# Kernel tuning notes

Measured on AMD Instinct MI355X. Metric: run time of the kernel, lower is better.

The kernel has to match this reference:

```python
import jax, jax.numpy as jnp
import numpy as np

REL_DIM = 64
HIDDEN = 128
IN_DIM = 7  # dist, dx, dy, color_diff(3), size_diff(1)


def setup_inputs() -> dict:
    key = jax.random.key(0)
    ks = jax.random.split(key, 8)
    B, N = 4, 512
    pos = jax.random.normal(ks[0], (B, N, 2), dtype=jnp.float32)
    color = jax.random.uniform(ks[1], (B, N, 3), dtype=jnp.float32)
    size = jax.random.uniform(ks[2], (B, N, 1), dtype=jnp.float32)
    # MLP params: Linear(7,128) -> GELU -> Linear(128,64), torch default init scale
    W1 = jax.random.normal(ks[3], (IN_DIM, HIDDEN), dtype=jnp.float32) / np.sqrt(IN_DIM)
    b1 = jax.random.normal(ks[4], (HIDDEN,), dtype=jnp.float32) * 0.01
    W2 = jax.random.normal(ks[5], (HIDDEN, REL_DIM), dtype=jnp.float32) / np.sqrt(HIDDEN)
    b2 = jax.random.normal(ks[6], (REL_DIM,), dtype=jnp.float32) * 0.01
    return {"pos": pos, "color": color, "size": size,
            "W1": W1, "b1": b1, "W2": W2, "b2": b2}


def reference(pos, color, size, W1, b1, W2, b2):
    # pos: (B,N,2), color: (B,N,3), size: (B,N,1)
    dx = pos[:, :, None, 0] - pos[:, None, :, 0]          # (B,N,N)
    dy = pos[:, :, None, 1] - pos[:, None, :, 1]          # (B,N,N)
    dist = jnp.sqrt(dx * dx + dy * dy + 1e-6)             # (B,N,N)
    color_diff = color[:, :, None, :] - color[:, None, :, :]  # (B,N,N,3)
    size_diff = size[:, :, None, :] - size[:, None, :, :]     # (B,N,N,1)
    geom = jnp.concatenate(
        [dist[..., None], dx[..., None], dy[..., None], color_diff, size_diff],
        axis=-1)                                          # (B,N,N,7)
    h = jax.nn.gelu(jnp.einsum('bijc,ch->bijh', geom, W1) + b1, approximate=False)
    rel = jnp.einsum('bijh,hr->bijr', h, W2) + b2          # (B,N,N,rel_dim)
    return rel
```

## Files before the change

### kernel.cpp

```cpp
#include <hip/hip_runtime.h>
#include <math.h>

#define NPTS 512
#define HID 128
#define RELD 64

typedef __attribute__((ext_vector_type(8))) short short8;
typedef __attribute__((ext_vector_type(4))) float f32x4;
typedef __attribute__((ext_vector_type(4))) int i32x4;

__global__ __launch_bounds__(256) void prep_tables(
    const float* __restrict__ pos, const float* __restrict__ color,
    const float* __restrict__ size, const float* __restrict__ W1,
    const float* __restrict__ b1, float* __restrict__ ui,
    unsigned short* __restrict__ uj, int npts)
{
  const int g = blockIdx.x * blockDim.x + threadIdx.x;
  const int k = g & (HID - 1), p = g >> 7;
  float v = pos[p * 2 + 0] * W1[1 * HID + k];
  v = fmaf(pos[p * 2 + 1], W1[2 * HID + k], v);
  v = fmaf(color[p * 3 + 0], W1[3 * HID + k], v);
  v = fmaf(color[p * 3 + 1], W1[4 * HID + k], v);
  v = fmaf(color[p * 3 + 2], W1[5 * HID + k], v);
  v = fmaf(size[p], W1[6 * HID + k], v);
  ui[g] = v + b1[k];
  const __bf16 vb = (__bf16)v;
  uj[((size_t)(k >> 3) * npts + p) * 8 + (k & 7)] = __builtin_bit_cast(unsigned short, vb);
}

__global__ __launch_bounds__(256) void relgeom_mfma5(
    const float* __restrict__ pos, const float* __restrict__ W1,
    const float* __restrict__ ui, const unsigned short* __restrict__ uj,
    const float* __restrict__ W2, const float* __restrict__ b2,
    float* __restrict__ out, int npts)
{
  __shared__ __align__(16) char lds[16384 + 4 * 4096];
  const int tid = threadIdx.x;
  const int lane = tid & 63, wid = tid >> 6;
  const int l15 = lane & 15, lq = lane >> 4, l3 = lane & 3;

#pragma unroll
  for (int n = 0; n < 32; ++n) {
    const int m = tid + 256 * n;
    const int k = m >> 6, r = m & 63;
    const __bf16 wb = (__bf16)W2[m];
    *(__bf16*)(lds + r * 256 + (((k >> 3) ^ (r & 7)) << 4) + (k & 7) * 2) = wb;
  }
  __syncthreads();

  const int bx = blockIdx.x;
  const int i  = (bx >> 1) & (NPTS - 1);
  const int b  = bx >> 10;
  const int pi = b * NPTS + i;
  const int j  = ((bx & 1) << 8) + tid;
  const int pj = b * NPTS + j;

  const float dx = pos[pi * 2 + 0] - pos[pj * 2 + 0];
  const float dy = pos[pi * 2 + 1] - pos[pj * 2 + 1];
  const float dist = sqrtf(fmaf(dx, dx, fmaf(dy, dy, 1e-6f)));

  const float* __restrict__ uirow = ui + (size_t)pi * HID;
  const float* __restrict__ w1d = W1;

  f32x4 acc[4][4];
#pragma unroll
  for (int rt = 0; rt < 4; ++rt) {
    const f32x4 bb = *(const f32x4*)(b2 + rt * 16 + lq * 4);
#pragma unroll
    for (int pt = 0; pt < 4; ++pt) acc[rt][pt] = bb;
  }

  char* const hbase = lds + 16384 + wid * 4096;

  for (int ks = 0; ks < 4; ++ks) {
    union { i32x4 v[4]; unsigned u[16]; } U;
#pragma unroll
    for (int d = 0; d < 4; ++d)
      U.v[d] = *(const i32x4*)(uj + ((size_t)(ks * 4 + d) * npts + pj) * 8);

    union { short s[32]; i32x4 v[4]; } hb;
#pragma unroll
    for (int kk = 0; kk < 32; ++kk) {
      const int k = ks * 32 + kk;
      const unsigned w = U.u[kk >> 1];
      const float ujf = __builtin_bit_cast(float, (kk & 1) ? (w & 0xffff0000u) : (w << 16));
      float h = fmaf(dist, w1d[k], uirow[k] - ujf);
      const float h2 = h * h;
      const float wq = fmaf(h2, -0.1029534f, -2.3022077f);
      const float ex = __builtin_amdgcn_exp2f(h * wq);
      const float gel = h * __builtin_amdgcn_rcpf(1.0f + ex);
      const __bf16 hbf = (__bf16)gel;
      hb.s[kk] = __builtin_bit_cast(short, hbf);
    }
#pragma unroll
    for (int d = 0; d < 4; ++d)
      *(i32x4*)(hbase + lane * 64 + ((d ^ l3) << 4)) = hb.v[d];

    short8 afr[4];
#pragma unroll
    for (int rt = 0; rt < 4; ++rt) {
      const int r = rt * 16 + l15;
      afr[rt] = *(const short8*)(lds + r * 256 + (((ks * 4 + lq) ^ (r & 7)) << 4));
    }
#pragma unroll
    for (int pt = 0; pt < 4; ++pt) {
      const int p = pt * 16 + l15;
      const short8 bfr = *(const short8*)(hbase + p * 64 + ((lq ^ (p & 3)) << 4));
#pragma unroll
      for (int rt = 0; rt < 4; ++rt)
        acc[rt][pt] = __builtin_amdgcn_mfma_f32_16x16x32_bf16(afr[rt], bfr, acc[rt][pt], 0, 0, 0);
    }
  }

  const int pbase = bx * 256 + wid * 64;
#pragma unroll
  for (int pt = 0; pt < 4; ++pt) {
#pragma unroll
    for (int rt = 0; rt < 4; ++rt) {
      const int c = (rt * 4 + lq) ^ l15;
      *(f32x4*)(hbase + l15 * 256 + (c & 15) * 16) = acc[rt][pt];
    }
    float* const ob = out + (size_t)(pbase + pt * 16) * RELD;
#pragma unroll
    for (int m = 0; m < 4; ++m) {
      const int g = m * 64 + lane;
      const int pr = g >> 4;
      const int c = (g & 15) ^ pr;
      const f32x4 v = *(const f32x4*)(hbase + pr * 256 + (c & 15) * 16);
      *(f32x4*)(ob + (size_t)g * 4) = v;
    }
  }
}

__global__ __launch_bounds__(256) void relgeom_mfma_fb(
    const float* __restrict__ pos, const float* __restrict__ color,
    const float* __restrict__ size, const float* __restrict__ W1,
    const float* __restrict__ b1, const float* __restrict__ W2,
    const float* __restrict__ b2, float* __restrict__ out)
{
  __shared__ __align__(16) char lds[16384 + 4 * 4096];
  const int tid = threadIdx.x;
  const int lane = tid & 63;
  const int wid = tid >> 6;
  const int l15 = lane & 15, lq = lane >> 4, l3 = lane & 3;
#pragma unroll
  for (int n = 0; n < 32; ++n) {
    const int m = tid + 256 * n;
    const int k = m >> 6, r = m & 63;
    const __bf16 wb = (__bf16)W2[m];
    *(__bf16*)(lds + r * 256 + (((k >> 3) ^ (r & 7)) << 4) + (k & 7) * 2) = wb;
  }
  __syncthreads();
  const int pbase = (blockIdx.x * 4 + wid) * 64;
  const int t = pbase + lane;
  const int j = t & (NPTS - 1);
  const int bi = t >> 9;
  const int i = bi & (NPTS - 1);
  const int b = bi >> 9;
  const int pi = b * NPTS + i, pj = b * NPTS + j;
  const float dx = pos[pi * 2 + 0] - pos[pj * 2 + 0];
  const float dy = pos[pi * 2 + 1] - pos[pj * 2 + 1];
  const float g0 = sqrtf(fmaf(dx, dx, fmaf(dy, dy, 1e-6f)));
  const float g3 = color[pi * 3 + 0] - color[pj * 3 + 0];
  const float g4 = color[pi * 3 + 1] - color[pj * 3 + 1];
  const float g5 = color[pi * 3 + 2] - color[pj * 3 + 2];
  const float g6 = size[pi] - size[pj];
  f32x4 acc[4][4];
#pragma unroll
  for (int nt = 0; nt < 4; ++nt) {
    const float bb = b2[nt * 16 + l15];
#pragma unroll
    for (int s = 0; s < 4; ++s) acc[s][nt] = (f32x4){bb, bb, bb, bb};
  }
  char* const hbase = lds + 16384 + wid * 4096;
  for (int ks = 0; ks < 4; ++ks) {
    union { short s[32]; i32x4 v[4]; } hb;
#pragma unroll
    for (int kk = 0; kk < 32; ++kk) {
      const int k = ks * 32 + kk;
      float h = b1[k];
      h = fmaf(g0, W1[0 * HID + k], h);
      h = fmaf(dx, W1[1 * HID + k], h);
      h = fmaf(dy, W1[2 * HID + k], h);
      h = fmaf(g3, W1[3 * HID + k], h);
      h = fmaf(g4, W1[4 * HID + k], h);
      h = fmaf(g5, W1[5 * HID + k], h);
      h = fmaf(g6, W1[6 * HID + k], h);
      const float h2 = h * h;
      const float wq = fmaf(h2, -0.1029534f, -2.3022077f);
      const float ex = __builtin_amdgcn_exp2f(h * wq);
      const float gel = h * __builtin_amdgcn_rcpf(1.0f + ex);
      const __bf16 hbf = (__bf16)gel;
      hb.s[kk] = __builtin_bit_cast(short, hbf);
    }
#pragma unroll
    for (int d = 0; d < 4; ++d)
      *(i32x4*)(hbase + lane * 64 + ((d ^ l3) << 4)) = hb.v[d];
    short8 bfr[4];
#pragma unroll
    for (int nt = 0; nt < 4; ++nt) {
      const int r = nt * 16 + l15;
      bfr[nt] = *(const short8*)(lds + r * 256 + (((ks * 4 + lq) ^ (r & 7)) << 4));
    }
#pragma unroll
    for (int s = 0; s < 4; ++s) {
      const short8 af = *(const short8*)(hbase + (s * 16 + l15) * 64 + ((lq ^ l3) << 4));
#pragma unroll
      for (int nt = 0; nt < 4; ++nt)
        acc[s][nt] = __builtin_amdgcn_mfma_f32_16x16x32_bf16(af, bfr[nt], acc[s][nt], 0, 0, 0);
    }
  }
  float* const op = out + (size_t)pbase * RELD;
#pragma unroll
  for (int s = 0; s < 4; ++s)
#pragma unroll
    for (int nt = 0; nt < 4; ++nt)
#pragma unroll
      for (int ri = 0; ri < 4; ++ri)
        op[(s * 16 + lq * 4 + ri) * RELD + nt * 16 + l15] = acc[s][nt][ri];
}

extern "C" void kernel_launch(void* const* d_in, const int* in_sizes, int n_in,
                              void* d_out, int out_size, void* d_ws, size_t ws_size,
                              hipStream_t stream) {
  const float* pos   = (const float*)d_in[0];
  const float* color = (const float*)d_in[1];
  const float* size  = (const float*)d_in[2];
  const float* W1    = (const float*)d_in[3];
  const float* b1    = (const float*)d_in[4];
  const float* W2    = (const float*)d_in[5];
  const float* b2    = (const float*)d_in[6];
  float* out = (float*)d_out;

  const int B = in_sizes[0] / (NPTS * 2);
  const int npts = B * NPTS;
  const long long pairs = (long long)B * NPTS * NPTS;

  const size_t ui_bytes = (size_t)npts * HID * sizeof(float);
  const size_t uj_bytes = (size_t)npts * HID * sizeof(unsigned short);

  if (ws_size >= ui_bytes + uj_bytes) {
    float* ui = (float*)d_ws;
    unsigned short* uj = (unsigned short*)((char*)d_ws + ui_bytes);
    prep_tables<<<npts * HID / 256, 256, 0, stream>>>(pos, color, size, W1, b1, ui, uj, npts);
    relgeom_mfma5<<<(int)(pairs / 256), 256, 0, stream>>>(pos, W1, ui, uj, W2, b2, out, npts);
  } else {
    relgeom_mfma_fb<<<(int)(pairs / 256), 256, 0, stream>>>(pos, color, size, W1, b1, W2, b2, out);
  }
}
```

Measured before the change: 77.09 us.

## Compute GELU activations directly in MFMA B-fragment layout, skipping LDS staging

Each lane now computes the hidden activations for the exact (pair, k-slice) elements it needs as the MFMA B operand: 8 k values for each of 4 pair columns. This removes the per-wave LDS write/read round trip of the hidden tile and shrinks LDS from 32KB to 16KB, which may raise occupancy. The epilogue reuses the W2 LDS region after a barrier. Each lane now computes sqrt for four pairs, and the loads of ui, W1 and uj are restructured into vector loads per k-slice. The gathered uj loads are less coalesced, and the fully unrolled ks loop may raise register pressure.

```diff
diff --git a/kernel.cpp b/kernel.cpp
--- a/kernel.cpp
+++ b/kernel.cpp
@@ -28,16 +28,16 @@
   uj[((size_t)(k >> 3) * npts + p) * 8 + (k & 7)] = __builtin_bit_cast(unsigned short, vb);
 }
 
-__global__ __launch_bounds__(256) void relgeom_mfma5(
+__global__ __launch_bounds__(256) void relgeom_mfma7(
     const float* __restrict__ pos, const float* __restrict__ W1,
     const float* __restrict__ ui, const unsigned short* __restrict__ uj,
     const float* __restrict__ W2, const float* __restrict__ b2,
     float* __restrict__ out, int npts)
 {
-  __shared__ __align__(16) char lds[16384 + 4 * 4096];
+  __shared__ __align__(16) char lds[16384];
   const int tid = threadIdx.x;
   const int lane = tid & 63, wid = tid >> 6;
-  const int l15 = lane & 15, lq = lane >> 4, l3 = lane & 3;
+  const int l15 = lane & 15, lq = lane >> 4;
 
 #pragma unroll
   for (int n = 0; n < 32; ++n) {
@@ -52,15 +52,21 @@
   const int i  = (bx >> 1) & (NPTS - 1);
   const int b  = bx >> 10;
   const int pi = b * NPTS + i;
-  const int j  = ((bx & 1) << 8) + tid;
-  const int pj = b * NPTS + j;
-
-  const float dx = pos[pi * 2 + 0] - pos[pj * 2 + 0];
-  const float dy = pos[pi * 2 + 1] - pos[pj * 2 + 1];
-  const float dist = sqrtf(fmaf(dx, dx, fmaf(dy, dy, 1e-6f)));
+  const int jc = ((bx & 1) << 8) + (wid << 6) + l15;
+  const int pj0 = b * NPTS + jc;
+
+  const float pix = pos[pi * 2 + 0], piy = pos[pi * 2 + 1];
+  float dist[4];
+  int pjs[4];
+#pragma unroll
+  for (int pt = 0; pt < 4; ++pt) {
+    pjs[pt] = pj0 + pt * 16;
+    const float dx = pix - pos[pjs[pt] * 2 + 0];
+    const float dy = piy - pos[pjs[pt] * 2 + 1];
+    dist[pt] = sqrtf(fmaf(dx, dx, fmaf(dy, dy, 1e-6f)));
+  }
 
   const float* __restrict__ uirow = ui + (size_t)pi * HID;
-  const float* __restrict__ w1d = W1;
 
   f32x4 acc[4][4];
 #pragma unroll
@@ -70,47 +76,53 @@
     for (int pt = 0; pt < 4; ++pt) acc[rt][pt] = bb;
   }
 
-  char* const hbase = lds + 16384 + wid * 4096;
-
+#pragma unroll
   for (int ks = 0; ks < 4; ++ks) {
-    union { i32x4 v[4]; unsigned u[16]; } U;
-#pragma unroll
-    for (int d = 0; d < 4; ++d)
-      U.v[d] = *(const i32x4*)(uj + ((size_t)(ks * 4 + d) * npts + pj) * 8);
-
-    union { short s[32]; i32x4 v[4]; } hb;
-#pragma unroll
-    for (int kk = 0; kk < 32; ++kk) {
-      const int k = ks * 32 + kk;
-      const unsigned w = U.u[kk >> 1];
-      const float ujf = __builtin_bit_cast(float, (kk & 1) ? (w & 0xffff0000u) : (w << 16));
-      float h = fmaf(dist, w1d[k], uirow[k] - ujf);
-      const float h2 = h * h;
-      const float wq = fmaf(h2, -0.1029534f, -2.3022077f);
-      const float ex = __builtin_amdgcn_exp2f(h * wq);
-      const float gel = h * __builtin_amdgcn_rcpf(1.0f + ex);
-      const __bf16 hbf = (__bf16)gel;
-      hb.s[kk] = __builtin_bit_cast(short, hbf);
-    }
-#pragma unroll
-    for (int d = 0; d < 4; ++d)
-      *(i32x4*)(hbase + lane * 64 + ((d ^ l3) << 4)) = hb.v[d];
+    const int kofs = ks * 32 + lq * 8;
+    const f32x4 uiA = *(const f32x4*)(uirow + kofs);
+    const f32x4 uiB = *(const f32x4*)(uirow + kofs + 4);
+    const f32x4 w1A = *(const f32x4*)(W1 + kofs);
+    const f32x4 w1B = *(const f32x4*)(W1 + kofs + 4);
+    const int o = ks * 4 + lq;
+
+    short8 bfr[4];
+#pragma unroll
+    for (int pt = 0; pt < 4; ++pt) {
+      union { i32x4 v; unsigned u[4]; } U;
+      U.v = *(const i32x4*)(uj + ((size_t)o * npts + pjs[pt]) * 8);
+      union { short s[8]; short8 v8; } hs;
+#pragma unroll
+      for (int e = 0; e < 8; ++e) {
+        const float uiv = (e < 4) ? uiA[e] : uiB[e - 4];
+        const float w1v = (e < 4) ? w1A[e] : w1B[e - 4];
+        const unsigned w = U.u[e >> 1];
+        const float ujf = __builtin_bit_cast(float, (e & 1) ? (w & 0xffff0000u) : (w << 16));
+        float h = fmaf(dist[pt], w1v, uiv - ujf);
+        const float h2 = h * h;
+        const float wq = fmaf(h2, -0.1029534f, -2.3022077f);
+        const float ex = __builtin_amdgcn_exp2f(h * wq);
+        const float gel = h * __builtin_amdgcn_rcpf(1.0f + ex);
+        const __bf16 hbf = (__bf16)gel;
+        hs.s[e] = __builtin_bit_cast(short, hbf);
+      }
+      bfr[pt] = hs.v8;
+    }
 
     short8 afr[4];
 #pragma unroll
     for (int rt = 0; rt < 4; ++rt) {
       const int r = rt * 16 + l15;
-      afr[rt] = *(const short8*)(lds + r * 256 + (((ks * 4 + lq) ^ (r & 7)) << 4));
-    }
-#pragma unroll
-    for (int pt = 0; pt < 4; ++pt) {
-      const int p = pt * 16 + l15;
-      const short8 bfr = *(const short8*)(hbase + p * 64 + ((lq ^ (p & 3)) << 4));
+      afr[rt] = *(const short8*)(lds + r * 256 + ((o ^ (r & 7)) << 4));
+    }
+#pragma unroll
+    for (int pt = 0; pt < 4; ++pt)
 #pragma unroll
       for (int rt = 0; rt < 4; ++rt)
-        acc[rt][pt] = __builtin_amdgcn_mfma_f32_16x16x32_bf16(afr[rt], bfr, acc[rt][pt], 0, 0, 0);
-    }
-  }
+        acc[rt][pt] = __builtin_amdgcn_mfma_f32_16x16x32_bf16(afr[rt], bfr[pt], acc[rt][pt], 0, 0, 0);
+  }
+
+  __syncthreads();
+  char* const ebase = lds + wid * 4096;
 
   const int pbase = bx * 256 + wid * 64;
 #pragma unroll
@@ -118,7 +130,7 @@
 #pragma unroll
     for (int rt = 0; rt < 4; ++rt) {
       const int c = (rt * 4 + lq) ^ l15;
-      *(f32x4*)(hbase + l15 * 256 + (c & 15) * 16) = acc[rt][pt];
+      *(f32x4*)(ebase + l15 * 256 + (c & 15) * 16) = acc[rt][pt];
     }
     float* const ob = out + (size_t)(pbase + pt * 16) * RELD;
 #pragma unroll
@@ -126,7 +138,7 @@
       const int g = m * 64 + lane;
       const int pr = g >> 4;
       const int c = (g & 15) ^ pr;
-      const f32x4 v = *(const f32x4*)(hbase + pr * 256 + (c & 15) * 16);
+      const f32x4 v = *(const f32x4*)(ebase + pr * 256 + (c & 15) * 16);
       *(f32x4*)(ob + (size_t)g * 4) = v;
     }
   }
@@ -168,9 +180,9 @@
   f32x4 acc[4][4];
 #pragma unroll
   for (int nt = 0; nt < 4; ++nt) {
-    const float bb = b2[nt * 16 + l15];
-#pragma unroll
-    for (int s = 0; s < 4; ++s) acc[s][nt] = (f32x4){bb, bb, bb, bb};
+    const float bbv = b2[nt * 16 + l15];
+#pragma unroll
+    for (int s = 0; s < 4; ++s) acc[s][nt] = (f32x4){bbv, bbv, bbv, bbv};
   }
   char* const hbase = lds + 16384 + wid * 4096;
   for (int ks = 0; ks < 4; ++ks) {
@@ -235,6 +247,7 @@
   const int B = in_sizes[0] / (NPTS * 2);
   const int npts = B * NPTS;
   const long long pairs = (long long)B * NPTS * NPTS;
+  const int ntiles = (int)(pairs / 256);
 
   const size_t ui_bytes = (size_t)npts * HID * sizeof(float);
   const size_t uj_bytes = (size_t)npts * HID * sizeof(unsigned short);
@@ -243,8 +256,8 @@
     float* ui = (float*)d_ws;
     unsigned short* uj = (unsigned short*)((char*)d_ws + ui_bytes);
     prep_tables<<<npts * HID / 256, 256, 0, stream>>>(pos, color, size, W1, b1, ui, uj, npts);
-    relgeom_mfma5<<<(int)(pairs / 256), 256, 0, stream>>>(pos, W1, ui, uj, W2, b2, out, npts);
+    relgeom_mfma7<<<ntiles, 256, 0, stream>>>(pos, W1, ui, uj, W2, b2, out, npts);
   } else {
-    relgeom_mfma_fb<<<(int)(pairs / 256), 256, 0, stream>>>(pos, color, size, W1, b1, W2, b2, out);
-  }
-}
+    relgeom_mfma_fb<<<ntiles, 256, 0, stream>>>(pos, color, size, W1, b1, W2, b2, out);
+  }
+}
```

Measured after the change: 114.5 us. 48.5% more time.
